# Performance work log

Measured on AMD Instinct MI355X. Metric: run time of the kernel, lower is better.

The kernel has to match this reference:

```python
import jax, jax.numpy as jnp
import numpy as np

TOP_K = 2  # top-k experts per token


def setup_inputs() -> dict:
    key = jax.random.key(0)
    k1, k2, k3, k4, k5 = jax.random.split(key, 5)
    B, S, D = 1, 2048, 2048
    E, F = 8, 1408
    scale = 0.02
    return {
        "hidden_states": jax.random.normal(k1, (B, S, D), dtype=jnp.float32),
        "gate_w": jax.random.normal(k2, (E, D), dtype=jnp.float32) * scale,
        "w_gate": jax.random.normal(k3, (E, D, F), dtype=jnp.float32) * scale,
        "w_up": jax.random.normal(k4, (E, D, F), dtype=jnp.float32) * scale,
        "w_down": jax.random.normal(k5, (E, F, D), dtype=jnp.float32) * scale,
    }


def reference(hidden_states, gate_w, w_gate, w_up, w_down):
    B, S, D = hidden_states.shape
    T = B * S
    x = hidden_states.reshape(T, D)  # flatten tokens, as in forward()

    # Router: combined gate built from per-rank 1-row gates -> [T, E] logits
    router_logits = jnp.einsum("td,ed->te", x, gate_w)
    routing_weights = jax.nn.softmax(router_logits, axis=-1)
    top_w, top_idx = jax.lax.top_k(routing_weights, TOP_K)  # [T, K]

    # Per-token combine weight for each expert (0 if expert not selected).
    # Equivalent to the one_hot expert_mask + index_add combine in the module.
    comb = jnp.zeros((T, gate_w.shape[0]), dtype=routing_weights.dtype)
    comb = comb.at[jnp.arange(T)[:, None], top_idx].add(top_w)  # [T, E]

    # Each expert is a Qwen2 MLP: down(silu(gate(x)) * up(x)).
    # (Dispatch/all-to-all collapses to dense-per-expert + masked combine
    #  on a single device; tokens with comb==0 contribute nothing.)
    g = jnp.einsum("td,edf->etf", x, w_gate)
    u = jnp.einsum("td,edf->etf", x, w_up)
    y = jnp.einsum("etf,efd->etd", jax.nn.silu(g) * u, w_down)  # [E, T, D]

    out = jnp.einsum("te,etd->td", comb, y)  # weighted combine (index_add)
    return out.reshape(B, S, D)
```

## Files before the change

kernel.cpp:

```cpp
#include <hip/hip_runtime.h>
#include <stdint.h>


#define TT 2048
#define DD 2048
#define FF 1408
#define NE 8
#define HROWS 5120
#define TRASH (2*TT)

typedef float f32x4 __attribute__((ext_vector_type(4)));
typedef short bf16x8 __attribute__((ext_vector_type(8)));

__device__ __forceinline__ unsigned short f2bf(float f) {
    unsigned int x = __float_as_uint(f);
    return (unsigned short)((x + 0x7fffu + ((x >> 16) & 1u)) >> 16);
}
__device__ __forceinline__ float bf2f(unsigned short u) {
    union { unsigned int i; float f; } v; v.i = ((unsigned int)u) << 16; return v.f;
}
__device__ __forceinline__ void gld16(const void* g, void* l) {
    __builtin_amdgcn_global_load_lds((const __attribute__((address_space(1))) void*)g,
                                     (__attribute__((address_space(3))) void*)l, 16, 0, 0);
}

__device__ __forceinline__ void treg(const float* __restrict__ src,
                                     unsigned short* __restrict__ dst,
                                     int R, int C, int r0, int c0) {
    const int lane = threadIdx.x & 63, w = threadIdx.x >> 6;
    const int bi = lane >> 3, bj = lane & 7;
    const int sr = r0 + (w & 1) * 64 + bi * 8;
    const int sc = c0 + (w >> 1) * 64 + bj * 8;
    float4 fa[8], fb[8];
#pragma unroll
    for (int k = 0; k < 8; ++k) {
        const float* p = src + (size_t)(sr + k) * C + sc;
        fa[k] = ((const float4*)p)[0];
        fb[k] = ((const float4*)p)[1];
    }
#pragma unroll
    for (int k = 0; k < 8; ++k) {
        uint4 ov; unsigned short* po = (unsigned short*)&ov;
#pragma unroll
        for (int l = 0; l < 8; ++l) {
            float v = (k < 4) ? ((const float*)&fa[l])[k]
                              : ((const float*)&fb[l])[k - 4];
            po[l] = f2bf(v);
        }
        *(uint4*)&dst[(size_t)(sc + k) * R + sr] = ov;
    }
}

__global__ void transpose_gu_kernel(const float* __restrict__ wg,
                                    const float* __restrict__ wu,
                                    unsigned short* __restrict__ WgT,
                                    unsigned short* __restrict__ WuT) {
    const int z = blockIdx.z;
    const float* src; unsigned short* dst;
    if (z < 8) { src = wg + (size_t)z * DD * FF;       dst = WgT + (size_t)z * FF * DD; }
    else       { src = wu + (size_t)(z - 8) * DD * FF; dst = WuT + (size_t)(z - 8) * FF * DD; }
    treg(src, dst, DD, FF, blockIdx.y * 128, blockIdx.x * 128);
}

__global__ void transpose_d_kernel(const float* __restrict__ wd,
                                   unsigned short* __restrict__ WdT) {
    const int z = blockIdx.z;
    treg(wd + (size_t)z * FF * DD, WdT + (size_t)z * DD * FF,
         FF, DD, blockIdx.y * 128, blockIdx.x * 128);
}

__global__ void router_kernel(const float* __restrict__ x,
                              const float* __restrict__ gw,
                              int* __restrict__ cnt,
                              int* __restrict__ tok,
                              float* __restrict__ wtv,
                              int* __restrict__ dstv,
                              unsigned short* __restrict__ xb,
                              int* __restrict__ basep,
                              int* __restrict__ cntpad) {
    __shared__ int s_last;
    __shared__ int sc[NE], sp[NE];

    const int wv = threadIdx.x >> 6, lane = threadIdx.x & 63;
    const int t = blockIdx.x * 4 + wv;
    float acc[NE];
#pragma unroll
    for (int e = 0; e < NE; ++e) acc[e] = 0.f;
    const float* xr = x + (size_t)t * DD;
    unsigned short* xbr = xb + (size_t)t * DD;
#pragma unroll
    for (int it = 0; it < DD / 256; ++it) {
        const int j = it * 256 + lane * 4;
        float4 xv = *(const float4*)(xr + j);
        short4 o;
        o.x = (short)f2bf(xv.x); o.y = (short)f2bf(xv.y);
        o.z = (short)f2bf(xv.z); o.w = (short)f2bf(xv.w);
        *(short4*)(xbr + j) = o;
#pragma unroll
        for (int e = 0; e < NE; ++e) {
            float4 g = *(const float4*)(gw + e * DD + j);
            acc[e] += xv.x * g.x + xv.y * g.y + xv.z * g.z + xv.w * g.w;
        }
    }
#pragma unroll
    for (int e = 0; e < NE; ++e) {
        float v = acc[e];
        v += __shfl_xor(v, 32); v += __shfl_xor(v, 16); v += __shfl_xor(v, 8);
        v += __shfl_xor(v, 4);  v += __shfl_xor(v, 2);  v += __shfl_xor(v, 1);
        acc[e] = v;
    }
    if (lane == 0) {
        float mx = acc[0];
#pragma unroll
        for (int e = 1; e < NE; ++e) mx = fmaxf(mx, acc[e]);
        float p[NE], s = 0.f;
#pragma unroll
        for (int e = 0; e < NE; ++e) { p[e] = __expf(acc[e] - mx); s += p[e]; }
        int i0 = 0;
#pragma unroll
        for (int e = 1; e < NE; ++e) if (p[e] > p[i0]) i0 = e;
        int i1 = (i0 == 0) ? 1 : 0;
#pragma unroll
        for (int e = 0; e < NE; ++e) if (e != i0 && p[e] > p[i1]) i1 = e;
        float inv = 1.f / s;
        int p0 = atomicAdd(&cnt[i0], 1);
        tok[i0 * TT + p0] = t; wtv[i0 * TT + p0] = p[i0] * inv; dstv[i0 * TT + p0] = 2 * t;
        int p1 = atomicAdd(&cnt[i1], 1);
        tok[i1 * TT + p1] = t; wtv[i1 * TT + p1] = p[i1] * inv; dstv[i1 * TT + p1] = 2 * t + 1;
    }

    __syncthreads();
    if (threadIdx.x == 0) {
        __threadfence();
        int d = atomicAdd(&cnt[NE], 1);
        s_last = (d == (TT / 4) - 1) ? 1 : 0;
    }
    __syncthreads();
    if (s_last) {
        if (threadIdx.x == 0) {
            int b = 0;
            for (int e = 0; e < NE; ++e) {
                int c = atomicAdd(&cnt[e], 0);
                int pd = (c + 127) & ~127;
                basep[e] = b; cntpad[e] = pd; sc[e] = c; sp[e] = pd; b += pd;
            }
        }
        __syncthreads();
        for (int e = 0; e < NE; ++e)
            for (int i = sc[e] + (int)threadIdx.x; i < sp[e]; i += 256) {
                tok[e * TT + i] = 0; wtv[e * TT + i] = 0.f; dstv[e * TT + i] = TRASH;
            }
    }
}

__launch_bounds__(256, 2)
__global__ void gemm1_kernel(const unsigned short* __restrict__ Xb,
                             const unsigned short* __restrict__ WgT,
                             const unsigned short* __restrict__ WuT,
                             const int* __restrict__ tok,
                             const int* __restrict__ base,
                             const int* __restrict__ cntpad,
                             unsigned short* __restrict__ H) {
    __shared__ unsigned short As[128 * 32];
    __shared__ unsigned short Bg[128 * 32];
    __shared__ unsigned short Bu[128 * 32];
    __shared__ int s_tok[128];

    const int e = blockIdx.z, rb = blockIdx.y, fb = blockIdx.x;
    const int cp = cntpad[e];
    if (rb * 128 >= cp) return;
    const int b0 = base[e];

    const int tid = threadIdx.x;
    if (tid < 128) s_tok[tid] = tok[e * TT + rb * 128 + tid];
    __syncthreads();

    const int w = tid >> 6, lane = tid & 63;
    const int r = lane & 15, q = lane >> 4;
    const int wm = w & 1, wn = w >> 1;

    const int srow = w * 32 + (lane >> 2);
    const int koff = (lane & 3) * 8;
    const unsigned short* ga0 = Xb + (size_t)s_tok[srow] * DD + koff;
    const unsigned short* ga1 = Xb + (size_t)s_tok[srow + 16] * DD + koff;
    const size_t wb = (size_t)e * FF * DD + (size_t)(fb * 128 + srow) * DD + koff;
    const unsigned short* gg0 = WgT + wb;
    const unsigned short* gg1 = WgT + wb + (size_t)16 * DD;
    const unsigned short* gu0 = WuT + wb;
    const unsigned short* gu1 = WuT + wb + (size_t)16 * DD;
    unsigned short* la0 = As + srow * 32 + koff;
    unsigned short* la1 = la0 + 512;
    unsigned short* lg0 = Bg + srow * 32 + koff;
    unsigned short* lg1 = lg0 + 512;
    unsigned short* lu0 = Bu + srow * 32 + koff;
    unsigned short* lu1 = lu0 + 512;

    f32x4 accg[4][4] = {};
    f32x4 accu[4][4] = {};

    for (int kt = 0; kt < DD / 32; ++kt) {
        gld16(ga0, la0); gld16(ga1, la1);
        gld16(gg0, lg0); gld16(gg1, lg1);
        gld16(gu0, lu0); gld16(gu1, lu1);
        ga0 += 32; ga1 += 32; gg0 += 32; gg1 += 32; gu0 += 32; gu1 += 32;
        __syncthreads();
        bf16x8 af[4], gf[4], uf[4];
#pragma unroll
        for (int m = 0; m < 4; ++m)
            af[m] = *(const bf16x8*)&As[(wm * 64 + m * 16 + r) * 32 + q * 8];
#pragma unroll
        for (int n = 0; n < 4; ++n) {
            gf[n] = *(const bf16x8*)&Bg[(wn * 64 + n * 16 + r) * 32 + q * 8];
            uf[n] = *(const bf16x8*)&Bu[(wn * 64 + n * 16 + r) * 32 + q * 8];
        }
#pragma unroll
        for (int m = 0; m < 4; ++m)
#pragma unroll
            for (int n = 0; n < 4; ++n) {
                accg[m][n] = __builtin_amdgcn_mfma_f32_16x16x32_bf16(af[m], gf[n], accg[m][n], 0, 0, 0);
                accu[m][n] = __builtin_amdgcn_mfma_f32_16x16x32_bf16(af[m], uf[n], accu[m][n], 0, 0, 0);
            }
        __syncthreads();
    }

    const size_t hr0 = (size_t)(b0 + rb * 128 + wm * 64);
#pragma unroll
    for (int m = 0; m < 4; ++m)
#pragma unroll
        for (int n = 0; n < 4; ++n)
#pragma unroll
            for (int rr = 0; rr < 4; ++rr) {
                float g = accg[m][n][rr], u = accu[m][n][rr];
                float h = (g / (1.f + __expf(-g))) * u;
                int row = m * 16 + q * 4 + rr;
                int col = fb * 128 + wn * 64 + n * 16 + r;
                H[(hr0 + row) * FF + col] = f2bf(h);
            }
}

__launch_bounds__(256, 2)
__global__ void gemm2_kernel(const unsigned short* __restrict__ H,
                             const unsigned short* __restrict__ WdT,
                             const float* __restrict__ wtv,
                             const int* __restrict__ dstv,
                             const int* __restrict__ base,
                             const int* __restrict__ cntpad,
                             unsigned short* __restrict__ Y) {
    __shared__ unsigned short As[128 * 32];
    __shared__ unsigned short Bs[128 * 32];
    __shared__ float s_w[128];
    __shared__ int s_d[128];

    const int e = blockIdx.z, rb = blockIdx.y, db = blockIdx.x;
    const int cp = cntpad[e];
    if (rb * 128 >= cp) return;
    const int b0 = base[e];

    const int tid = threadIdx.x;
    if (tid < 128) {
        int idx = e * TT + rb * 128 + tid;
        s_w[tid] = wtv[idx]; s_d[tid] = dstv[idx];
    }
    __syncthreads();

    const int w = tid >> 6, lane = tid & 63;
    const int r = lane & 15, q = lane >> 4;
    const int wm = w & 1, wn = w >> 1;

    const int srow = w * 32 + (lane >> 2);
    const int koff = (lane & 3) * 8;
    const unsigned short* ga0 = H + (size_t)(b0 + rb * 128 + srow) * FF + koff;
    const unsigned short* ga1 = ga0 + (size_t)16 * FF;
    const unsigned short* gb0 = WdT + (size_t)e * DD * FF + (size_t)(db * 128 + srow) * FF + koff;
    const unsigned short* gb1 = gb0 + (size_t)16 * FF;
    unsigned short* la0 = As + srow * 32 + koff;
    unsigned short* la1 = la0 + 512;
    unsigned short* lb0 = Bs + srow * 32 + koff;
    unsigned short* lb1 = lb0 + 512;

    f32x4 acc[4][4] = {};

    for (int kt = 0; kt < FF / 32; ++kt) {
        gld16(ga0, la0); gld16(ga1, la1);
        gld16(gb0, lb0); gld16(gb1, lb1);
        ga0 += 32; ga1 += 32; gb0 += 32; gb1 += 32;
        __syncthreads();
        bf16x8 af[4], bf[4];
#pragma unroll
        for (int m = 0; m < 4; ++m)
            af[m] = *(const bf16x8*)&As[(wm * 64 + m * 16 + r) * 32 + q * 8];
#pragma unroll
        for (int n = 0; n < 4; ++n)
            bf[n] = *(const bf16x8*)&Bs[(wn * 64 + n * 16 + r) * 32 + q * 8];
#pragma unroll
        for (int m = 0; m < 4; ++m)
#pragma unroll
            for (int n = 0; n < 4; ++n)
                acc[m][n] = __builtin_amdgcn_mfma_f32_16x16x32_bf16(af[m], bf[n], acc[m][n], 0, 0, 0);
        __syncthreads();
    }

#pragma unroll
    for (int m = 0; m < 4; ++m)
#pragma unroll
        for (int n = 0; n < 4; ++n)
#pragma unroll
            for (int rr = 0; rr < 4; ++rr) {
                int row = wm * 64 + m * 16 + q * 4 + rr;
                int col = db * 128 + wn * 64 + n * 16 + r;
                float v = s_w[row] * acc[m][n][rr];
                Y[(size_t)s_d[row] * DD + col] = f2bf(v);
            }
}

__global__ void combine_kernel(const unsigned short* __restrict__ Y,
                               float* __restrict__ out) {
    const int t = blockIdx.x;
    const int d = threadIdx.x * 8;
    uint4 a = *(const uint4*)(Y + (size_t)(2 * t) * DD + d);
    uint4 b = *(const uint4*)(Y + (size_t)(2 * t + 1) * DD + d);
    const unsigned short* pa = (const unsigned short*)&a;
    const unsigned short* pb = (const unsigned short*)&b;
    float4 o0, o1;
    o0.x = bf2f(pa[0]) + bf2f(pb[0]);  o0.y = bf2f(pa[1]) + bf2f(pb[1]);
    o0.z = bf2f(pa[2]) + bf2f(pb[2]);  o0.w = bf2f(pa[3]) + bf2f(pb[3]);
    o1.x = bf2f(pa[4]) + bf2f(pb[4]);  o1.y = bf2f(pa[5]) + bf2f(pb[5]);
    o1.z = bf2f(pa[6]) + bf2f(pb[6]);  o1.w = bf2f(pa[7]) + bf2f(pb[7]);
    float* op = out + (size_t)t * DD + d;
    ((float4*)op)[0] = o0;
    ((float4*)op)[1] = o1;
}

extern "C" void kernel_launch(void* const* d_in, const int* in_sizes, int n_in,
                              void* d_out, int out_size, void* d_ws, size_t ws_size,
                              hipStream_t stream) {
    const float* x      = (const float*)d_in[0];
    const float* gw     = (const float*)d_in[1];
    const float* w_gate = (const float*)d_in[2];
    const float* w_up   = (const float*)d_in[3];
    const float* w_down = (const float*)d_in[4];
    float* out = (float*)d_out;

    uint8_t* ws = (uint8_t*)d_ws;
    size_t off = 0;
    auto alloc = [&](size_t bytes) -> void* {
        void* p = ws + off;
        off = (off + bytes + 255) & ~(size_t)255;
        return p;
    };
    int*   cnt    = (int*)  alloc((NE + 1) * 4);
    int*   basep  = (int*)  alloc(NE * 4);
    int*   cntpad = (int*)  alloc(NE * 4);
    int*   tok    = (int*)  alloc((size_t)NE * TT * 4);
    float* wtv    = (float*)alloc((size_t)NE * TT * 4);
    int*   dstv   = (int*)  alloc((size_t)NE * TT * 4);
    unsigned short* Xb  = (unsigned short*)alloc((size_t)TT * DD * 2);
    unsigned short* Hb  = (unsigned short*)alloc((size_t)HROWS * FF * 2);
    unsigned short* Yb  = (unsigned short*)alloc((size_t)(2 * TT + 8) * DD * 2);
    unsigned short* WT  = (unsigned short*)alloc((size_t)2 * NE * FF * DD * 2);
    unsigned short* WgT = WT;
    unsigned short* WuT = WT + (size_t)NE * FF * DD;
    unsigned short* WdT = WT;
    (void)ws_size; (void)in_sizes; (void)n_in; (void)out_size;

    hipMemsetAsync(cnt, 0, (NE + 1) * 4, stream);
    transpose_gu_kernel<<<dim3(11, 16, 16), 256, 0, stream>>>(w_gate, w_up, WgT, WuT);
    router_kernel<<<dim3(TT / 4), 256, 0, stream>>>(x, gw, cnt, tok, wtv, dstv, Xb, basep, cntpad);
    gemm1_kernel<<<dim3(FF / 128, TT / 128, NE), 256, 0, stream>>>(Xb, WgT, WuT, tok, basep, cntpad, Hb);
    transpose_d_kernel<<<dim3(16, 11, 8), 256, 0, stream>>>(w_down, WdT);
    gemm2_kernel<<<dim3(DD / 128, TT / 128, NE), 256, 0, stream>>>(Hb, WdT, wtv, dstv, basep, cntpad, Yb);
    combine_kernel<<<dim3(TT), 256, 0, stream>>>(Yb, out);
}
```

Measured before the change: 508.6 us.

## Replace weight transposes with plain bf16 conversion and LDS transpose reads

The weight preprocessing no longer transposes the fp32 weights. It only converts them to bf16 in their original [D,F] and [F,D] layouts with simple coalesced elementwise kernels. Both GEMMs now load K-major weight tiles into LDS and use ds_read_b64_tr_b16 to produce the transposed MFMA B operands. This removes the strided transpose writes, in exchange for row-strided global loads per k-tile and an explicit lgkmcnt wait plus sched barrier in the inner loop.

```diff
diff --git a/kernel.cpp b/kernel.cpp
--- a/kernel.cpp
+++ b/kernel.cpp
@@ -11,6 +11,8 @@
 
 typedef float f32x4 __attribute__((ext_vector_type(4)));
 typedef short bf16x8 __attribute__((ext_vector_type(8)));
+typedef short bf16x4 __attribute__((ext_vector_type(4)));
+typedef const __attribute__((address_space(3))) unsigned short* lds_cp;
 
 __device__ __forceinline__ unsigned short f2bf(float f) {
     unsigned int x = __float_as_uint(f);
@@ -24,49 +26,38 @@
                                      (__attribute__((address_space(3))) void*)l, 16, 0, 0);
 }
 
-__device__ __forceinline__ void treg(const float* __restrict__ src,
-                                     unsigned short* __restrict__ dst,
-                                     int R, int C, int r0, int c0) {
-    const int lane = threadIdx.x & 63, w = threadIdx.x >> 6;
-    const int bi = lane >> 3, bj = lane & 7;
-    const int sr = r0 + (w & 1) * 64 + bi * 8;
-    const int sc = c0 + (w >> 1) * 64 + bj * 8;
-    float4 fa[8], fb[8];
-#pragma unroll
-    for (int k = 0; k < 8; ++k) {
-        const float* p = src + (size_t)(sr + k) * C + sc;
-        fa[k] = ((const float4*)p)[0];
-        fb[k] = ((const float4*)p)[1];
-    }
-#pragma unroll
-    for (int k = 0; k < 8; ++k) {
-        uint4 ov; unsigned short* po = (unsigned short*)&ov;
-#pragma unroll
-        for (int l = 0; l < 8; ++l) {
-            float v = (k < 4) ? ((const float*)&fa[l])[k]
-                              : ((const float*)&fb[l])[k - 4];
-            po[l] = f2bf(v);
-        }
-        *(uint4*)&dst[(size_t)(sc + k) * R + sr] = ov;
-    }
-}
-
-__global__ void transpose_gu_kernel(const float* __restrict__ wg,
-                                    const float* __restrict__ wu,
-                                    unsigned short* __restrict__ WgT,
-                                    unsigned short* __restrict__ WuT) {
+#define TR16(d, p, imm) \
+    asm volatile("ds_read_b64_tr_b16 %0, %1 offset:" imm : "=&v"(d) : "v"(p))
+
+__global__ void convert_gu_kernel(const float* __restrict__ wg,
+                                  const float* __restrict__ wu,
+                                  unsigned short* __restrict__ G,
+                                  unsigned short* __restrict__ U) {
     const int z = blockIdx.z;
-    const float* src; unsigned short* dst;
-    if (z < 8) { src = wg + (size_t)z * DD * FF;       dst = WgT + (size_t)z * FF * DD; }
-    else       { src = wu + (size_t)(z - 8) * DD * FF; dst = WuT + (size_t)(z - 8) * FF * DD; }
-    treg(src, dst, DD, FF, blockIdx.y * 128, blockIdx.x * 128);
-}
-
-__global__ void transpose_d_kernel(const float* __restrict__ wd,
-                                   unsigned short* __restrict__ WdT) {
+    const float* s; unsigned short* d;
+    if (z < NE) { s = wg + (size_t)z * DD * FF;        d = G + (size_t)z * DD * FF; }
+    else        { s = wu + (size_t)(z - NE) * DD * FF; d = U + (size_t)(z - NE) * DD * FF; }
+    const size_t i = ((size_t)blockIdx.x * 256 + threadIdx.x) * 8;
+    float4 a = *(const float4*)(s + i);
+    float4 b = *(const float4*)(s + i + 4);
+    uint4 o; unsigned short* po = (unsigned short*)&o;
+    po[0] = f2bf(a.x); po[1] = f2bf(a.y); po[2] = f2bf(a.z); po[3] = f2bf(a.w);
+    po[4] = f2bf(b.x); po[5] = f2bf(b.y); po[6] = f2bf(b.z); po[7] = f2bf(b.w);
+    *(uint4*)(d + i) = o;
+}
+
+__global__ void convert_d_kernel(const float* __restrict__ wd,
+                                 unsigned short* __restrict__ W) {
     const int z = blockIdx.z;
-    treg(wd + (size_t)z * FF * DD, WdT + (size_t)z * DD * FF,
-         FF, DD, blockIdx.y * 128, blockIdx.x * 128);
+    const float* s = wd + (size_t)z * FF * DD;
+    unsigned short* d = W + (size_t)z * FF * DD;
+    const size_t i = ((size_t)blockIdx.x * 256 + threadIdx.x) * 8;
+    float4 a = *(const float4*)(s + i);
+    float4 b = *(const float4*)(s + i + 4);
+    uint4 o; unsigned short* po = (unsigned short*)&o;
+    po[0] = f2bf(a.x); po[1] = f2bf(a.y); po[2] = f2bf(a.z); po[3] = f2bf(a.w);
+    po[4] = f2bf(b.x); po[5] = f2bf(b.y); po[6] = f2bf(b.z); po[7] = f2bf(b.w);
+    *(uint4*)(d + i) = o;
 }
 
 __global__ void router_kernel(const float* __restrict__ x,
@@ -153,10 +144,11 @@
     }
 }
 
+
 __launch_bounds__(256, 2)
 __global__ void gemm1_kernel(const unsigned short* __restrict__ Xb,
-                             const unsigned short* __restrict__ WgT,
-                             const unsigned short* __restrict__ WuT,
+                             const unsigned short* __restrict__ Wg,
+                             const unsigned short* __restrict__ Wu,
                              const int* __restrict__ tok,
                              const int* __restrict__ base,
                              const int* __restrict__ cntpad,
@@ -183,17 +175,24 @@
     const int koff = (lane & 3) * 8;
     const unsigned short* ga0 = Xb + (size_t)s_tok[srow] * DD + koff;
     const unsigned short* ga1 = Xb + (size_t)s_tok[srow + 16] * DD + koff;
-    const size_t wb = (size_t)e * FF * DD + (size_t)(fb * 128 + srow) * DD + koff;
-    const unsigned short* gg0 = WgT + wb;
-    const unsigned short* gg1 = WgT + wb + (size_t)16 * DD;
-    const unsigned short* gu0 = WuT + wb;
-    const unsigned short* gu1 = WuT + wb + (size_t)16 * DD;
     unsigned short* la0 = As + srow * 32 + koff;
     unsigned short* la1 = la0 + 512;
-    unsigned short* lg0 = Bg + srow * 32 + koff;
-    unsigned short* lg1 = lg0 + 512;
-    unsigned short* lu0 = Bu + srow * 32 + koff;
-    unsigned short* lu1 = lu0 + 512;
+
+    const int s0 = tid, s1 = tid + 256;
+    const int k0 = 4 * (s0 >> 6) + ((s0 >> 1) & 3), f0 = 16 * ((s0 >> 3) & 7) + 8 * (s0 & 1);
+    const int k1 = 4 * (s1 >> 6) + ((s1 >> 1) & 3), f1 = 16 * ((s1 >> 3) & 7) + 8 * (s1 & 1);
+    const size_t wb = (size_t)e * DD * FF + (size_t)fb * 128;
+    const unsigned short* gg0 = Wg + wb + (size_t)k0 * FF + f0;
+    const unsigned short* gg1 = Wg + wb + (size_t)k1 * FF + f1;
+    const unsigned short* gu0 = Wu + wb + (size_t)k0 * FF + f0;
+    const unsigned short* gu1 = Wu + wb + (size_t)k1 * FF + f1;
+    unsigned short* lg0 = Bg + s0 * 8;
+    unsigned short* lg1 = Bg + s1 * 8;
+    unsigned short* lu0 = Bu + s0 * 8;
+    unsigned short* lu1 = Bu + s1 * 8;
+
+    lds_cp bg = (lds_cp)Bg + (q * 1024 + wn * 256 + 4 * r);
+    lds_cp bu = (lds_cp)Bu + (q * 1024 + wn * 256 + 4 * r);
 
     f32x4 accg[4][4] = {};
     f32x4 accu[4][4] = {};
@@ -202,16 +201,32 @@
         gld16(ga0, la0); gld16(ga1, la1);
         gld16(gg0, lg0); gld16(gg1, lg1);
         gld16(gu0, lu0); gld16(gu1, lu1);
-        ga0 += 32; ga1 += 32; gg0 += 32; gg1 += 32; gu0 += 32; gu1 += 32;
+        ga0 += 32; ga1 += 32;
+        gg0 += 32 * FF; gg1 += 32 * FF; gu0 += 32 * FF; gu1 += 32 * FF;
         __syncthreads();
-        bf16x8 af[4], gf[4], uf[4];
+
+        bf16x8 af[4];
 #pragma unroll
         for (int m = 0; m < 4; ++m)
             af[m] = *(const bf16x8*)&As[(wm * 64 + m * 16 + r) * 32 + q * 8];
+
+        bf16x4 gA[8], uA[8];
+        TR16(gA[0], bg, "0");    TR16(gA[1], bg, "1024");
+        TR16(gA[2], bg, "128");  TR16(gA[3], bg, "1152");
+        TR16(gA[4], bg, "256");  TR16(gA[5], bg, "1280");
+        TR16(gA[6], bg, "384");  TR16(gA[7], bg, "1408");
+        TR16(uA[0], bu, "0");    TR16(uA[1], bu, "1024");
+        TR16(uA[2], bu, "128");  TR16(uA[3], bu, "1152");
+        TR16(uA[4], bu, "256");  TR16(uA[5], bu, "1280");
+        TR16(uA[6], bu, "384");  TR16(uA[7], bu, "1408");
+        asm volatile("s_waitcnt lgkmcnt(0)" ::: "memory");
+        __builtin_amdgcn_sched_barrier(0);
+
+        bf16x8 gf[4], uf[4];
 #pragma unroll
         for (int n = 0; n < 4; ++n) {
-            gf[n] = *(const bf16x8*)&Bg[(wn * 64 + n * 16 + r) * 32 + q * 8];
-            uf[n] = *(const bf16x8*)&Bu[(wn * 64 + n * 16 + r) * 32 + q * 8];
+            gf[n] = __builtin_shufflevector(gA[2 * n], gA[2 * n + 1], 0, 1, 2, 3, 4, 5, 6, 7);
+            uf[n] = __builtin_shufflevector(uA[2 * n], uA[2 * n + 1], 0, 1, 2, 3, 4, 5, 6, 7);
         }
 #pragma unroll
         for (int m = 0; m < 4; ++m)
@@ -240,7 +255,7 @@
 
 __launch_bounds__(256, 2)
 __global__ void gemm2_kernel(const unsigned short* __restrict__ H,
-                             const unsigned short* __restrict__ WdT,
+                             const unsigned short* __restrict__ Wd,
                              const float* __restrict__ wtv,
                              const int* __restrict__ dstv,
                              const int* __restrict__ base,
@@ -271,27 +286,46 @@
     const int koff = (lane & 3) * 8;
     const unsigned short* ga0 = H + (size_t)(b0 + rb * 128 + srow) * FF + koff;
     const unsigned short* ga1 = ga0 + (size_t)16 * FF;
-    const unsigned short* gb0 = WdT + (size_t)e * DD * FF + (size_t)(db * 128 + srow) * FF + koff;
-    const unsigned short* gb1 = gb0 + (size_t)16 * FF;
     unsigned short* la0 = As + srow * 32 + koff;
     unsigned short* la1 = la0 + 512;
-    unsigned short* lb0 = Bs + srow * 32 + koff;
-    unsigned short* lb1 = lb0 + 512;
+
+    const int s0 = tid, s1 = tid + 256;
+    const int k0 = 4 * (s0 >> 6) + ((s0 >> 1) & 3), f0 = 16 * ((s0 >> 3) & 7) + 8 * (s0 & 1);
+    const int k1 = 4 * (s1 >> 6) + ((s1 >> 1) & 3), f1 = 16 * ((s1 >> 3) & 7) + 8 * (s1 & 1);
+    const size_t wb = (size_t)e * FF * DD + (size_t)db * 128;
+    const unsigned short* gb0 = Wd + wb + (size_t)k0 * DD + f0;
+    const unsigned short* gb1 = Wd + wb + (size_t)k1 * DD + f1;
+    unsigned short* lb0 = Bs + s0 * 8;
+    unsigned short* lb1 = Bs + s1 * 8;
+
+    lds_cp bb = (lds_cp)Bs + (q * 1024 + wn * 256 + 4 * r);
 
     f32x4 acc[4][4] = {};
 
     for (int kt = 0; kt < FF / 32; ++kt) {
         gld16(ga0, la0); gld16(ga1, la1);
         gld16(gb0, lb0); gld16(gb1, lb1);
-        ga0 += 32; ga1 += 32; gb0 += 32; gb1 += 32;
+        ga0 += 32; ga1 += 32;
+        gb0 += 32 * DD; gb1 += 32 * DD;
         __syncthreads();
-        bf16x8 af[4], bf[4];
+
+        bf16x8 af[4];
 #pragma unroll
         for (int m = 0; m < 4; ++m)
             af[m] = *(const bf16x8*)&As[(wm * 64 + m * 16 + r) * 32 + q * 8];
+
+        bf16x4 bA[8];
+        TR16(bA[0], bb, "0");    TR16(bA[1], bb, "1024");
+        TR16(bA[2], bb, "128");  TR16(bA[3], bb, "1152");
+        TR16(bA[4], bb, "256");  TR16(bA[5], bb, "1280");
+        TR16(bA[6], bb, "384");  TR16(bA[7], bb, "1408");
+        asm volatile("s_waitcnt lgkmcnt(0)" ::: "memory");
+        __builtin_amdgcn_sched_barrier(0);
+
+        bf16x8 bf[4];
 #pragma unroll
         for (int n = 0; n < 4; ++n)
-            bf[n] = *(const bf16x8*)&Bs[(wn * 64 + n * 16 + r) * 32 + q * 8];
+            bf[n] = __builtin_shufflevector(bA[2 * n], bA[2 * n + 1], 0, 1, 2, 3, 4, 5, 6, 7);
 #pragma unroll
         for (int m = 0; m < 4; ++m)
 #pragma unroll
@@ -358,16 +392,16 @@
     unsigned short* Hb  = (unsigned short*)alloc((size_t)HROWS * FF * 2);
     unsigned short* Yb  = (unsigned short*)alloc((size_t)(2 * TT + 8) * DD * 2);
     unsigned short* WT  = (unsigned short*)alloc((size_t)2 * NE * FF * DD * 2);
-    unsigned short* WgT = WT;
-    unsigned short* WuT = WT + (size_t)NE * FF * DD;
-    unsigned short* WdT = WT;
+    unsigned short* WgB = WT;
+    unsigned short* WuB = WT + (size_t)NE * FF * DD;
+    unsigned short* WdB = WT;
     (void)ws_size; (void)in_sizes; (void)n_in; (void)out_size;
 
     hipMemsetAsync(cnt, 0, (NE + 1) * 4, stream);
-    transpose_gu_kernel<<<dim3(11, 16, 16), 256, 0, stream>>>(w_gate, w_up, WgT, WuT);
+    convert_gu_kernel<<<dim3(DD * FF / 2048, 1, 2 * NE), 256, 0, stream>>>(w_gate, w_up, WgB, WuB);
     router_kernel<<<dim3(TT / 4), 256, 0, stream>>>(x, gw, cnt, tok, wtv, dstv, Xb, basep, cntpad);
-    gemm1_kernel<<<dim3(FF / 128, TT / 128, NE), 256, 0, stream>>>(Xb, WgT, WuT, tok, basep, cntpad, Hb);
-    transpose_d_kernel<<<dim3(16, 11, 8), 256, 0, stream>>>(w_down, WdT);
-    gemm2_kernel<<<dim3(DD / 128, TT / 128, NE), 256, 0, stream>>>(Hb, WdT, wtv, dstv, basep, cntpad, Yb);
+    gemm1_kernel<<<dim3(FF / 128, TT / 128, NE), 256, 0, stream>>>(Xb, WgB, WuB, tok, basep, cntpad, Hb);
+    convert_d_kernel<<<dim3(FF * DD / 2048, 1, NE), 256, 0, stream>>>(w_down, WdB);
+    gemm2_kernel<<<dim3(DD / 128, TT / 128, NE), 256, 0, stream>>>(Hb, WdB, wtv, dstv, basep, cntpad, Yb);
     combine_kernel<<<dim3(TT), 256, 0, stream>>>(Yb, out);
 }
```

Result: faster. 497.6 us (-2.1%).
